# Optimization experiments

Measured on AMD Instinct MI355X. Metric: run time of the kernel, lower is better.

Reference implementation:

```python
import jax, jax.numpy as jnp
import numpy as np

EPS = 1e-08


def setup_inputs() -> dict:
    key = jax.random.key(0)
    k1, k2, k3 = jax.random.split(key, 3)
    N = 4000000
    x = jax.random.normal(k1, (N, 3), dtype=jnp.float32)
    x_gt = jax.random.normal(k2, (N, 3), dtype=jnp.float32)
    weights = jax.random.uniform(k3, (N,), dtype=jnp.float32)
    return {"x": x, "x_gt": x_gt, "weights": weights}


def reference(x, x_gt, weights):
    # weights: [N] -> [N, 1]
    w = weights[:, None]
    weight_sum = w.sum() + EPS
    mu = (w * x).sum(axis=0, keepdims=True) / weight_sum        # [1, 3]
    mu_gt = (w * x_gt).sum(axis=0, keepdims=True) / weight_sum  # [1, 3]
    x_c = x - mu
    x_gt_c = x_gt - mu_gt
    sw = jnp.sqrt(w)
    # H = (sqrt(w)*x_c)^T @ (sqrt(w)*x_gt_c)  -> [3, 3]
    H = jnp.einsum('ni,nj->ij', sw * x_c, sw * x_gt_c)
    U, S, Vt = jnp.linalg.svd(H)
    R = U @ Vt  # == U @ V.T with V = Vt.T
    det_R = jnp.linalg.det(R)
    # Reflection fix: R = U @ diag(1,1,d) @ Vt with d = -1 if det < 0
    d = jnp.where(det_R < 0, -1.0, 1.0).astype(R.dtype)
    F = jnp.array([1.0, 1.0, 0.0], dtype=R.dtype) + jnp.array([0.0, 0.0, 1.0], dtype=R.dtype) * d
    R = (U * F[None, :]) @ Vt
    # x_aligned = (R @ x_gt_c^T)^T + mu = x_gt_c @ R^T + mu
    x_aligned = x_gt_c @ R.T + mu
    return jax.lax.stop_gradient(x_aligned)
```

## Files before the change

### kernel.cpp

```cpp
#include <hip/hip_runtime.h>
#include <math.h>

#define BLK 256

__global__ __launch_bounds__(BLK) void wra_reduce(
    const float* __restrict__ x, const float* __restrict__ g,
    const float* __restrict__ w, float* __restrict__ partials,
    int n4, int n, int ntiles)
{
    __shared__ float4 xs[768];
    __shared__ float4 gs[768];
    __shared__ float4 ws[256];

    float a[16];
#pragma unroll
    for (int i = 0; i < 16; ++i) a[i] = 0.f;

    const float4* __restrict__ x4 = (const float4*)x;
    const float4* __restrict__ g4 = (const float4*)g;
    const float4* __restrict__ w4 = (const float4*)w;

    const int tid = threadIdx.x;
    const int totc = 3 * n4;

    for (int t = blockIdx.x; t < ntiles; t += gridDim.x) {
        const int cb = t * 768;
        const int wb = t * 256;
#pragma unroll
        for (int k = 0; k < 3; ++k) {
            int c = cb + tid + 256 * k;
            float4 xv = make_float4(0.f, 0.f, 0.f, 0.f);
            float4 gv = xv;
            if (c < totc) { xv = x4[c]; gv = g4[c]; }
            xs[tid + 256 * k] = xv;
            gs[tid + 256 * k] = gv;
        }
        {
            int wc = wb + tid;
            ws[tid] = (wc < n4) ? w4[wc] : make_float4(0.f, 0.f, 0.f, 0.f);
        }
        __syncthreads();

        float4 xa = xs[3 * tid + 0], xb = xs[3 * tid + 1], xc = xs[3 * tid + 2];
        float4 ga = gs[3 * tid + 0], gb = gs[3 * tid + 1], gc = gs[3 * tid + 2];
        float4 wv = ws[tid];

        float px[4] = {xa.x, xa.w, xb.z, xc.y};
        float py[4] = {xa.y, xb.x, xb.w, xc.z};
        float pz[4] = {xa.z, xb.y, xc.x, xc.w};
        float qx[4] = {ga.x, ga.w, gb.z, gc.y};
        float qy[4] = {ga.y, gb.x, gb.w, gc.z};
        float qz[4] = {ga.z, gb.y, gc.x, gc.w};
        float wt[4] = {wv.x, wv.y, wv.z, wv.w};
#pragma unroll
        for (int k = 0; k < 4; ++k) {
            float wk = wt[k];
            float wpx = wk * px[k], wpy = wk * py[k], wpz = wk * pz[k];
            a[0] += wk;
            a[1] += wpx;         a[2] += wpy;         a[3] += wpz;
            a[4] += wk * qx[k];  a[5] += wk * qy[k];  a[6] += wk * qz[k];
            a[7]  += wpx * qx[k]; a[8]  += wpx * qy[k]; a[9]  += wpx * qz[k];
            a[10] += wpy * qx[k]; a[11] += wpy * qy[k]; a[12] += wpy * qz[k];
            a[13] += wpz * qx[k]; a[14] += wpz * qy[k]; a[15] += wpz * qz[k];
        }
        __syncthreads();
    }

    if (blockIdx.x == 0 && tid == 0) {
        for (int r = n4 * 4; r < n; ++r) {
            float wk = w[r];
            float X = x[3 * r], Y = x[3 * r + 1], Z = x[3 * r + 2];
            float Gx = g[3 * r], Gy = g[3 * r + 1], Gz = g[3 * r + 2];
            float wpx = wk * X, wpy = wk * Y, wpz = wk * Z;
            a[0] += wk;
            a[1] += wpx;      a[2] += wpy;      a[3] += wpz;
            a[4] += wk * Gx;  a[5] += wk * Gy;  a[6] += wk * Gz;
            a[7]  += wpx * Gx; a[8]  += wpx * Gy; a[9]  += wpx * Gz;
            a[10] += wpy * Gx; a[11] += wpy * Gy; a[12] += wpy * Gz;
            a[13] += wpz * Gx; a[14] += wpz * Gy; a[15] += wpz * Gz;
        }
    }

#pragma unroll
    for (int i = 0; i < 16; ++i) {
        float v = a[i];
        for (int off = 32; off > 0; off >>= 1) v += __shfl_down(v, off, 64);
        a[i] = v;
    }
    __shared__ float red[4][16];
    int lane = tid & 63;
    int wid  = tid >> 6;
    if (lane == 0) {
#pragma unroll
        for (int i = 0; i < 16; ++i) red[wid][i] = a[i];
    }
    __syncthreads();
    if (tid < 16) {
        float s = red[0][tid] + red[1][tid] + red[2][tid] + red[3][tid];
        partials[blockIdx.x * 16 + tid] = s;
    }
}

__global__ __launch_bounds__(64) void wra_solve(
    const float* __restrict__ partials, int nb, float* __restrict__ rt)
{
    int lane = threadIdx.x;
    double acc[16];
#pragma unroll
    for (int i = 0; i < 16; ++i) acc[i] = 0.0;
    for (int b = lane; b < nb; b += 64) {
#pragma unroll
        for (int i = 0; i < 16; ++i) acc[i] += (double)partials[b * 16 + i];
    }
#pragma unroll
    for (int i = 0; i < 16; ++i) {
        double v = acc[i];
        for (int off = 32; off > 0; off >>= 1) v += __shfl_down(v, off, 64);
        acc[i] = v;
    }
    if (lane != 0) return;

    double Sw = acc[0];
    double Sx[3] = {acc[1], acc[2], acc[3]};
    double Sg[3] = {acc[4], acc[5], acc[6]};
    double Hr[3][3];
    for (int i = 0; i < 3; ++i)
        for (int j = 0; j < 3; ++j) Hr[i][j] = acc[7 + i * 3 + j];

    double W = Sw + 1e-8;
    double mu[3], mg[3];
    for (int i = 0; i < 3; ++i) { mu[i] = Sx[i] / W; mg[i] = Sg[i] / W; }

    double H[3][3];
    for (int i = 0; i < 3; ++i)
        for (int j = 0; j < 3; ++j)
            H[i][j] = Hr[i][j] - mu[i] * Sg[j] - mg[j] * Sx[i] + mu[i] * mg[j] * Sw;

    double A[3][3];
    for (int i = 0; i < 3; ++i)
        for (int j = 0; j < 3; ++j) {
            double s = 0.0;
            for (int k = 0; k < 3; ++k) s += H[k][i] * H[k][j];
            A[i][j] = s;
        }

    double V[3][3] = {{1,0,0},{0,1,0},{0,0,1}};
    const int pr[3] = {0, 0, 1}, qr[3] = {1, 2, 2};
    for (int sweep = 0; sweep < 25; ++sweep) {
        for (int r = 0; r < 3; ++r) {
            int p = pr[r], q = qr[r];
            double apq = A[p][q];
            if (fabs(apq) < 1e-30) continue;
            double tau = (A[q][q] - A[p][p]) / (2.0 * apq);
            double t = (tau >= 0 ? 1.0 : -1.0) / (fabs(tau) + sqrt(1.0 + tau * tau));
            double c = 1.0 / sqrt(1.0 + t * t), s = t * c;
            for (int k = 0; k < 3; ++k) {
                double akp = A[k][p], akq = A[k][q];
                A[k][p] = c * akp - s * akq;
                A[k][q] = s * akp + c * akq;
            }
            for (int k = 0; k < 3; ++k) {
                double apk = A[p][k], aqk = A[q][k];
                A[p][k] = c * apk - s * aqk;
                A[q][k] = s * apk + c * aqk;
            }
            for (int k = 0; k < 3; ++k) {
                double vkp = V[k][p], vkq = V[k][q];
                V[k][p] = c * vkp - s * vkq;
                V[k][q] = s * vkp + c * vkq;
            }
        }
    }
    double lam[3] = {A[0][0], A[1][1], A[2][2]};

    int idx[3] = {0, 1, 2};
    if (lam[idx[0]] < lam[idx[1]]) { int t = idx[0]; idx[0] = idx[1]; idx[1] = t; }
    if (lam[idx[1]] < lam[idx[2]]) { int t = idx[1]; idx[1] = idx[2]; idx[2] = t; }
    if (lam[idx[0]] < lam[idx[1]]) { int t = idx[0]; idx[0] = idx[1]; idx[1] = t; }

    double Vs[3][3], U[3][3];
    for (int k = 0; k < 3; ++k) {
        int c0 = idx[k];
        double l = lam[c0] > 1e-30 ? lam[c0] : 1e-30;
        double inv = 1.0 / sqrt(l);
        for (int i = 0; i < 3; ++i) Vs[i][k] = V[i][c0];
        for (int i = 0; i < 3; ++i) {
            double s = 0.0;
            for (int j = 0; j < 3; ++j) s += H[i][j] * Vs[j][k];
            U[i][k] = s * inv;
        }
    }

    double detH = H[0][0] * (H[1][1] * H[2][2] - H[1][2] * H[2][1])
                - H[0][1] * (H[1][0] * H[2][2] - H[1][2] * H[2][0])
                + H[0][2] * (H[1][0] * H[2][1] - H[1][1] * H[2][0]);
    double d = (detH < 0.0) ? -1.0 : 1.0;

    double R[3][3];
    for (int i = 0; i < 3; ++i)
        for (int j = 0; j < 3; ++j)
            R[i][j] = U[i][0] * Vs[j][0] + U[i][1] * Vs[j][1] + d * U[i][2] * Vs[j][2];

    double tv[3];
    for (int i = 0; i < 3; ++i)
        tv[i] = mu[i] - (R[i][0] * mg[0] + R[i][1] * mg[1] + R[i][2] * mg[2]);

    for (int i = 0; i < 3; ++i)
        for (int j = 0; j < 3; ++j) rt[i * 3 + j] = (float)R[i][j];
    for (int i = 0; i < 3; ++i) rt[9 + i] = (float)tv[i];
}

__global__ __launch_bounds__(BLK) void wra_apply(
    const float* __restrict__ g, const float* __restrict__ rt,
    float* __restrict__ out, int n4, int n, int ntiles)
{
    __shared__ float4 buf[768];

    float R00 = rt[0], R01 = rt[1], R02 = rt[2];
    float R10 = rt[3], R11 = rt[4], R12 = rt[5];
    float R20 = rt[6], R21 = rt[7], R22 = rt[8];
    float t0 = rt[9], t1 = rt[10], t2 = rt[11];

    const float4* __restrict__ g4 = (const float4*)g;
    float4* __restrict__ o4 = (float4*)out;

    const int tid = threadIdx.x;
    const int totc = 3 * n4;

    for (int t = blockIdx.x; t < ntiles; t += gridDim.x) {
        const int cb = t * 768;
#pragma unroll
        for (int k = 0; k < 3; ++k) {
            int c = cb + tid + 256 * k;
            if (c < totc) buf[tid + 256 * k] = g4[c];
        }
        __syncthreads();

        float4 ga = buf[3 * tid + 0], gb = buf[3 * tid + 1], gc = buf[3 * tid + 2];
        float qx0 = ga.x, qy0 = ga.y, qz0 = ga.z;
        float qx1 = ga.w, qy1 = gb.x, qz1 = gb.y;
        float qx2 = gb.z, qy2 = gb.w, qz2 = gc.x;
        float qx3 = gc.y, qy3 = gc.z, qz3 = gc.w;

        float ox0 = R00*qx0 + R01*qy0 + R02*qz0 + t0;
        float oy0 = R10*qx0 + R11*qy0 + R12*qz0 + t1;
        float oz0 = R20*qx0 + R21*qy0 + R22*qz0 + t2;
        float ox1 = R00*qx1 + R01*qy1 + R02*qz1 + t0;
        float oy1 = R10*qx1 + R11*qy1 + R12*qz1 + t1;
        float oz1 = R20*qx1 + R21*qy1 + R22*qz1 + t2;
        float ox2 = R00*qx2 + R01*qy2 + R02*qz2 + t0;
        float oy2 = R10*qx2 + R11*qy2 + R12*qz2 + t1;
        float oz2 = R20*qx2 + R21*qy2 + R22*qz2 + t2;
        float ox3 = R00*qx3 + R01*qy3 + R02*qz3 + t0;
        float oy3 = R10*qx3 + R11*qy3 + R12*qz3 + t1;
        float oz3 = R20*qx3 + R21*qy3 + R22*qz3 + t2;

        buf[3 * tid + 0] = make_float4(ox0, oy0, oz0, ox1);
        buf[3 * tid + 1] = make_float4(oy1, oz1, ox2, oy2);
        buf[3 * tid + 2] = make_float4(oz2, ox3, oy3, oz3);
        __syncthreads();

#pragma unroll
        for (int k = 0; k < 3; ++k) {
            int c = cb + tid + 256 * k;
            if (c < totc) o4[c] = buf[tid + 256 * k];
        }
        __syncthreads();
    }

    int gtid = blockIdx.x * blockDim.x + threadIdx.x;
    int gstr = gridDim.x * blockDim.x;
    for (int r = n4 * 4 + gtid; r < n; r += gstr) {
        float Gx = g[3 * r], Gy = g[3 * r + 1], Gz = g[3 * r + 2];
        out[3 * r + 0] = R00 * Gx + R01 * Gy + R02 * Gz + t0;
        out[3 * r + 1] = R10 * Gx + R11 * Gy + R12 * Gz + t1;
        out[3 * r + 2] = R20 * Gx + R21 * Gy + R22 * Gz + t2;
    }
}

extern "C" void kernel_launch(void* const* d_in, const int* in_sizes, int n_in,
                              void* d_out, int out_size, void* d_ws, size_t ws_size,
                              hipStream_t stream)
{
    const float* x = (const float*)d_in[0];
    const float* g = (const float*)d_in[1];
    const float* w = (const float*)d_in[2];
    float* out = (float*)d_out;

    int n = in_sizes[2];
    int n4 = n / 4;
    int ntiles = (n4 + 255) / 256;
    if (ntiles < 1) ntiles = 1;

    int nbr = 1024;
    int maxnb = (int)((ws_size / sizeof(float) - 12) / 16);
    if (nbr > maxnb) nbr = maxnb;
    if (nbr > ntiles) nbr = ntiles;
    if (nbr < 1) nbr = 1;

    float* partials = (float*)d_ws;
    float* rt = partials + (size_t)nbr * 16;

    wra_reduce<<<nbr, BLK, 0, stream>>>(x, g, w, partials, n4, n, ntiles);
    wra_solve<<<1, 64, 0, stream>>>(partials, nbr, rt);

    int nba = ntiles < 2048 ? ntiles : 2048;
    wra_apply<<<nba, BLK, 0, stream>>>(g, rt, out, n4, n, ntiles);
}
```

Measured before the change: 56.88 us.

## Prefetch next tile into registers while computing current tile from shared memory

Restructures the grid-stride reduction loop so the global loads for the next tile are issued into registers before the current tile is processed from shared memory, then stored to shared memory after a barrier. This software pipelining is meant to hide global memory latency behind the accumulation math in a bandwidth-bound reduction. It costs extra registers for the prefetch buffers, which may lower occupancy, and adds a second barrier per iteration.

```diff
diff --git a/kernel.cpp b/kernel.cpp
--- a/kernel.cpp
+++ b/kernel.cpp
@@ -22,48 +22,75 @@
 
     const int tid = threadIdx.x;
     const int totc = 3 * n4;
-
-    for (int t = blockIdx.x; t < ntiles; t += gridDim.x) {
+    const float4 z4 = make_float4(0.f, 0.f, 0.f, 0.f);
+
+    int t = blockIdx.x;
+    {
+        float4 rx[3], rg[3], rw;
         const int cb = t * 768;
-        const int wb = t * 256;
 #pragma unroll
         for (int k = 0; k < 3; ++k) {
             int c = cb + tid + 256 * k;
-            float4 xv = make_float4(0.f, 0.f, 0.f, 0.f);
-            float4 gv = xv;
-            if (c < totc) { xv = x4[c]; gv = g4[c]; }
-            xs[tid + 256 * k] = xv;
-            gs[tid + 256 * k] = gv;
-        }
+            rx[k] = z4; rg[k] = z4;
+            if (c < totc) { rx[k] = x4[c]; rg[k] = g4[c]; }
+        }
+        int wc = t * 256 + tid;
+        rw = (wc < n4) ? w4[wc] : z4;
+#pragma unroll
+        for (int k = 0; k < 3; ++k) { xs[tid + 256 * k] = rx[k]; gs[tid + 256 * k] = rg[k]; }
+        ws[tid] = rw;
+    }
+    __syncthreads();
+
+    while (t < ntiles) {
+        const int tn = t + gridDim.x;
+        const bool havenext = (tn < ntiles);
+        float4 px[3], pg[3], pw;
+        if (havenext) {
+            const int cb = tn * 768;
+#pragma unroll
+            for (int k = 0; k < 3; ++k) {
+                int c = cb + tid + 256 * k;
+                px[k] = z4; pg[k] = z4;
+                if (c < totc) { px[k] = x4[c]; pg[k] = g4[c]; }
+            }
+            int wc = tn * 256 + tid;
+            pw = (wc < n4) ? w4[wc] : z4;
+        }
+
         {
-            int wc = wb + tid;
-            ws[tid] = (wc < n4) ? w4[wc] : make_float4(0.f, 0.f, 0.f, 0.f);
-        }
-        __syncthreads();
-
-        float4 xa = xs[3 * tid + 0], xb = xs[3 * tid + 1], xc = xs[3 * tid + 2];
-        float4 ga = gs[3 * tid + 0], gb = gs[3 * tid + 1], gc = gs[3 * tid + 2];
-        float4 wv = ws[tid];
-
-        float px[4] = {xa.x, xa.w, xb.z, xc.y};
-        float py[4] = {xa.y, xb.x, xb.w, xc.z};
-        float pz[4] = {xa.z, xb.y, xc.x, xc.w};
-        float qx[4] = {ga.x, ga.w, gb.z, gc.y};
-        float qy[4] = {ga.y, gb.x, gb.w, gc.z};
-        float qz[4] = {ga.z, gb.y, gc.x, gc.w};
-        float wt[4] = {wv.x, wv.y, wv.z, wv.w};
-#pragma unroll
-        for (int k = 0; k < 4; ++k) {
-            float wk = wt[k];
-            float wpx = wk * px[k], wpy = wk * py[k], wpz = wk * pz[k];
-            a[0] += wk;
-            a[1] += wpx;         a[2] += wpy;         a[3] += wpz;
-            a[4] += wk * qx[k];  a[5] += wk * qy[k];  a[6] += wk * qz[k];
-            a[7]  += wpx * qx[k]; a[8]  += wpx * qy[k]; a[9]  += wpx * qz[k];
-            a[10] += wpy * qx[k]; a[11] += wpy * qy[k]; a[12] += wpy * qz[k];
-            a[13] += wpz * qx[k]; a[14] += wpz * qy[k]; a[15] += wpz * qz[k];
-        }
-        __syncthreads();
+            float4 xa = xs[3 * tid + 0], xb = xs[3 * tid + 1], xc = xs[3 * tid + 2];
+            float4 ga = gs[3 * tid + 0], gb = gs[3 * tid + 1], gc = gs[3 * tid + 2];
+            float4 wv = ws[tid];
+
+            float pxc[4] = {xa.x, xa.w, xb.z, xc.y};
+            float pyc[4] = {xa.y, xb.x, xb.w, xc.z};
+            float pzc[4] = {xa.z, xb.y, xc.x, xc.w};
+            float qxc[4] = {ga.x, ga.w, gb.z, gc.y};
+            float qyc[4] = {ga.y, gb.x, gb.w, gc.z};
+            float qzc[4] = {ga.z, gb.y, gc.x, gc.w};
+            float wt[4]  = {wv.x, wv.y, wv.z, wv.w};
+#pragma unroll
+            for (int k = 0; k < 4; ++k) {
+                float wk = wt[k];
+                float wpx = wk * pxc[k], wpy = wk * pyc[k], wpz = wk * pzc[k];
+                a[0] += wk;
+                a[1] += wpx;          a[2] += wpy;          a[3] += wpz;
+                a[4] += wk * qxc[k];  a[5] += wk * qyc[k];  a[6] += wk * qzc[k];
+                a[7]  += wpx * qxc[k]; a[8]  += wpx * qyc[k]; a[9]  += wpx * qzc[k];
+                a[10] += wpy * qxc[k]; a[11] += wpy * qyc[k]; a[12] += wpy * qzc[k];
+                a[13] += wpz * qxc[k]; a[14] += wpz * qyc[k]; a[15] += wpz * qzc[k];
+            }
+        }
+        __syncthreads();
+
+        if (havenext) {
+#pragma unroll
+            for (int k = 0; k < 3; ++k) { xs[tid + 256 * k] = px[k]; gs[tid + 256 * k] = pg[k]; }
+            ws[tid] = pw;
+        }
+        __syncthreads();
+        t = tn;
     }
 
     if (blockIdx.x == 0 && tid == 0) {
```

Measured after the change: 56.81 us. No clear change (-0.1%).

## Load reduce inputs directly into registers with nontemporal loads and 2x unroll

Applied to the files above, without the earlier changes.

The reduction kernel drops its shared-memory staging and barriers. Each thread now loads its own three float4 of x and g plus one float4 of w straight into registers, with a two-iteration unroll to keep more loads in flight. x and w use nontemporal loads while g uses normal loads, presumably so g stays in cache for the apply pass. The apply kernel writes its output with nontemporal stores, and the reduce grid grows from 1024 to 2048 blocks. The trade-off is strided per-thread 48-byte accesses, which coalesce less well than the old staged loads.

```diff
diff --git a/kernel.cpp b/kernel.cpp
--- a/kernel.cpp
+++ b/kernel.cpp
@@ -1,76 +1,86 @@
 #include <hip/hip_runtime.h>
 #include <math.h>
 
+typedef float f32x4 __attribute__((ext_vector_type(4)));
+
 #define BLK 256
+
+__device__ __forceinline__ void accum4(
+    float a[16], f32x4 xa, f32x4 xb, f32x4 xc,
+    f32x4 ga, f32x4 gb, f32x4 gc, f32x4 wv)
+{
+    float px[4] = {xa.x, xa.w, xb.z, xc.y};
+    float py[4] = {xa.y, xb.x, xb.w, xc.z};
+    float pz[4] = {xa.z, xb.y, xc.x, xc.w};
+    float qx[4] = {ga.x, ga.w, gb.z, gc.y};
+    float qy[4] = {ga.y, gb.x, gb.w, gc.z};
+    float qz[4] = {ga.z, gb.y, gc.x, gc.w};
+    float wt[4] = {wv.x, wv.y, wv.z, wv.w};
+#pragma unroll
+    for (int k = 0; k < 4; ++k) {
+        float wk = wt[k];
+        float wpx = wk * px[k], wpy = wk * py[k], wpz = wk * pz[k];
+        a[0] += wk;
+        a[1] += wpx;         a[2] += wpy;         a[3] += wpz;
+        a[4] += wk * qx[k];  a[5] += wk * qy[k];  a[6] += wk * qz[k];
+        a[7]  += wpx * qx[k]; a[8]  += wpx * qy[k]; a[9]  += wpx * qz[k];
+        a[10] += wpy * qx[k]; a[11] += wpy * qy[k]; a[12] += wpy * qz[k];
+        a[13] += wpz * qx[k]; a[14] += wpz * qy[k]; a[15] += wpz * qz[k];
+    }
+}
 
 __global__ __launch_bounds__(BLK) void wra_reduce(
     const float* __restrict__ x, const float* __restrict__ g,
     const float* __restrict__ w, float* __restrict__ partials,
-    int n4, int n, int ntiles)
-{
-    __shared__ float4 xs[768];
-    __shared__ float4 gs[768];
-    __shared__ float4 ws[256];
-
+    int n4, int n)
+{
     float a[16];
 #pragma unroll
     for (int i = 0; i < 16; ++i) a[i] = 0.f;
 
-    const float4* __restrict__ x4 = (const float4*)x;
-    const float4* __restrict__ g4 = (const float4*)g;
-    const float4* __restrict__ w4 = (const float4*)w;
-
-    const int tid = threadIdx.x;
-    const int totc = 3 * n4;
-
-    for (int t = blockIdx.x; t < ntiles; t += gridDim.x) {
-        const int cb = t * 768;
-        const int wb = t * 256;
-#pragma unroll
-        for (int k = 0; k < 3; ++k) {
-            int c = cb + tid + 256 * k;
-            float4 xv = make_float4(0.f, 0.f, 0.f, 0.f);
-            float4 gv = xv;
-            if (c < totc) { xv = x4[c]; gv = g4[c]; }
-            xs[tid + 256 * k] = xv;
-            gs[tid + 256 * k] = gv;
-        }
-        {
-            int wc = wb + tid;
-            ws[tid] = (wc < n4) ? w4[wc] : make_float4(0.f, 0.f, 0.f, 0.f);
-        }
-        __syncthreads();
-
-        float4 xa = xs[3 * tid + 0], xb = xs[3 * tid + 1], xc = xs[3 * tid + 2];
-        float4 ga = gs[3 * tid + 0], gb = gs[3 * tid + 1], gc = gs[3 * tid + 2];
-        float4 wv = ws[tid];
-
-        float px[4] = {xa.x, xa.w, xb.z, xc.y};
-        float py[4] = {xa.y, xb.x, xb.w, xc.z};
-        float pz[4] = {xa.z, xb.y, xc.x, xc.w};
-        float qx[4] = {ga.x, ga.w, gb.z, gc.y};
-        float qy[4] = {ga.y, gb.x, gb.w, gc.z};
-        float qz[4] = {ga.z, gb.y, gc.x, gc.w};
-        float wt[4] = {wv.x, wv.y, wv.z, wv.w};
-#pragma unroll
-        for (int k = 0; k < 4; ++k) {
-            float wk = wt[k];
-            float wpx = wk * px[k], wpy = wk * py[k], wpz = wk * pz[k];
-            a[0] += wk;
-            a[1] += wpx;         a[2] += wpy;         a[3] += wpz;
-            a[4] += wk * qx[k];  a[5] += wk * qy[k];  a[6] += wk * qz[k];
-            a[7]  += wpx * qx[k]; a[8]  += wpx * qy[k]; a[9]  += wpx * qz[k];
-            a[10] += wpy * qx[k]; a[11] += wpy * qy[k]; a[12] += wpy * qz[k];
-            a[13] += wpz * qx[k]; a[14] += wpz * qy[k]; a[15] += wpz * qz[k];
-        }
-        __syncthreads();
-    }
-
-    if (blockIdx.x == 0 && tid == 0) {
+    const f32x4* __restrict__ x4 = (const f32x4*)x;
+    const f32x4* __restrict__ g4 = (const f32x4*)g;
+    const f32x4* __restrict__ w4 = (const f32x4*)w;
+
+    int tid = blockIdx.x * blockDim.x + threadIdx.x;
+    int stride = gridDim.x * blockDim.x;
+
+    int i = tid;
+    for (; i + stride < n4; i += 2 * stride) {
+        int j = i + stride;
+        f32x4 xa0 = __builtin_nontemporal_load(&x4[3*i+0]);
+        f32x4 xb0 = __builtin_nontemporal_load(&x4[3*i+1]);
+        f32x4 xc0 = __builtin_nontemporal_load(&x4[3*i+2]);
+        f32x4 ga0 = g4[3*i+0];
+        f32x4 gb0 = g4[3*i+1];
+        f32x4 gc0 = g4[3*i+2];
+        f32x4 wv0 = __builtin_nontemporal_load(&w4[i]);
+        f32x4 xa1 = __builtin_nontemporal_load(&x4[3*j+0]);
+        f32x4 xb1 = __builtin_nontemporal_load(&x4[3*j+1]);
+        f32x4 xc1 = __builtin_nontemporal_load(&x4[3*j+2]);
+        f32x4 ga1 = g4[3*j+0];
+        f32x4 gb1 = g4[3*j+1];
+        f32x4 gc1 = g4[3*j+2];
+        f32x4 wv1 = __builtin_nontemporal_load(&w4[j]);
+        accum4(a, xa0, xb0, xc0, ga0, gb0, gc0, wv0);
+        accum4(a, xa1, xb1, xc1, ga1, gb1, gc1, wv1);
+    }
+    for (; i < n4; i += stride) {
+        f32x4 xa = __builtin_nontemporal_load(&x4[3*i+0]);
+        f32x4 xb = __builtin_nontemporal_load(&x4[3*i+1]);
+        f32x4 xc = __builtin_nontemporal_load(&x4[3*i+2]);
+        f32x4 ga = g4[3*i+0];
+        f32x4 gb = g4[3*i+1];
+        f32x4 gc = g4[3*i+2];
+        f32x4 wv = __builtin_nontemporal_load(&w4[i]);
+        accum4(a, xa, xb, xc, ga, gb, gc, wv);
+    }
+
+    if (blockIdx.x == 0 && threadIdx.x == 0) {
         for (int r = n4 * 4; r < n; ++r) {
             float wk = w[r];
-            float X = x[3 * r], Y = x[3 * r + 1], Z = x[3 * r + 2];
-            float Gx = g[3 * r], Gy = g[3 * r + 1], Gz = g[3 * r + 2];
+            float X = x[3*r], Y = x[3*r+1], Z = x[3*r+2];
+            float Gx = g[3*r], Gy = g[3*r+1], Gz = g[3*r+2];
             float wpx = wk * X, wpy = wk * Y, wpz = wk * Z;
             a[0] += wk;
             a[1] += wpx;      a[2] += wpy;      a[3] += wpz;
@@ -82,22 +92,23 @@
     }
 
 #pragma unroll
-    for (int i = 0; i < 16; ++i) {
-        float v = a[i];
+    for (int i2 = 0; i2 < 16; ++i2) {
+        float v = a[i2];
         for (int off = 32; off > 0; off >>= 1) v += __shfl_down(v, off, 64);
-        a[i] = v;
+        a[i2] = v;
     }
     __shared__ float red[4][16];
-    int lane = tid & 63;
-    int wid  = tid >> 6;
+    int lane = threadIdx.x & 63;
+    int wid  = threadIdx.x >> 6;
     if (lane == 0) {
 #pragma unroll
-        for (int i = 0; i < 16; ++i) red[wid][i] = a[i];
+        for (int i2 = 0; i2 < 16; ++i2) red[wid][i2] = a[i2];
     }
     __syncthreads();
-    if (tid < 16) {
-        float s = red[0][tid] + red[1][tid] + red[2][tid] + red[3][tid];
-        partials[blockIdx.x * 16 + tid] = s;
+    if (threadIdx.x < 16) {
+        float s = red[0][threadIdx.x] + red[1][threadIdx.x]
+                + red[2][threadIdx.x] + red[3][threadIdx.x];
+        partials[blockIdx.x * 16 + threadIdx.x] = s;
     }
 }
 
@@ -214,15 +225,15 @@
     const float* __restrict__ g, const float* __restrict__ rt,
     float* __restrict__ out, int n4, int n, int ntiles)
 {
-    __shared__ float4 buf[768];
+    __shared__ f32x4 buf[768];
 
     float R00 = rt[0], R01 = rt[1], R02 = rt[2];
     float R10 = rt[3], R11 = rt[4], R12 = rt[5];
     float R20 = rt[6], R21 = rt[7], R22 = rt[8];
     float t0 = rt[9], t1 = rt[10], t2 = rt[11];
 
-    const float4* __restrict__ g4 = (const float4*)g;
-    float4* __restrict__ o4 = (float4*)out;
+    const f32x4* __restrict__ g4 = (const f32x4*)g;
+    f32x4* __restrict__ o4 = (f32x4*)out;
 
     const int tid = threadIdx.x;
     const int totc = 3 * n4;
@@ -236,34 +247,35 @@
         }
         __syncthreads();
 
-        float4 ga = buf[3 * tid + 0], gb = buf[3 * tid + 1], gc = buf[3 * tid + 2];
+        f32x4 ga = buf[3 * tid + 0], gb = buf[3 * tid + 1], gc = buf[3 * tid + 2];
         float qx0 = ga.x, qy0 = ga.y, qz0 = ga.z;
         float qx1 = ga.w, qy1 = gb.x, qz1 = gb.y;
         float qx2 = gb.z, qy2 = gb.w, qz2 = gc.x;
         float qx3 = gc.y, qy3 = gc.z, qz3 = gc.w;
 
-        float ox0 = R00*qx0 + R01*qy0 + R02*qz0 + t0;
-        float oy0 = R10*qx0 + R11*qy0 + R12*qz0 + t1;
-        float oz0 = R20*qx0 + R21*qy0 + R22*qz0 + t2;
-        float ox1 = R00*qx1 + R01*qy1 + R02*qz1 + t0;
-        float oy1 = R10*qx1 + R11*qy1 + R12*qz1 + t1;
-        float oz1 = R20*qx1 + R21*qy1 + R22*qz1 + t2;
-        float ox2 = R00*qx2 + R01*qy2 + R02*qz2 + t0;
-        float oy2 = R10*qx2 + R11*qy2 + R12*qz2 + t1;
-        float oz2 = R20*qx2 + R21*qy2 + R22*qz2 + t2;
-        float ox3 = R00*qx3 + R01*qy3 + R02*qz3 + t0;
-        float oy3 = R10*qx3 + R11*qy3 + R12*qz3 + t1;
-        float oz3 = R20*qx3 + R21*qy3 + R22*qz3 + t2;
-
-        buf[3 * tid + 0] = make_float4(ox0, oy0, oz0, ox1);
-        buf[3 * tid + 1] = make_float4(oy1, oz1, ox2, oy2);
-        buf[3 * tid + 2] = make_float4(oz2, ox3, oy3, oz3);
+        f32x4 r0, r1, r2;
+        r0.x = R00*qx0 + R01*qy0 + R02*qz0 + t0;
+        r0.y = R10*qx0 + R11*qy0 + R12*qz0 + t1;
+        r0.z = R20*qx0 + R21*qy0 + R22*qz0 + t2;
+        r0.w = R00*qx1 + R01*qy1 + R02*qz1 + t0;
+        r1.x = R10*qx1 + R11*qy1 + R12*qz1 + t1;
+        r1.y = R20*qx1 + R21*qy1 + R22*qz1 + t2;
+        r1.z = R00*qx2 + R01*qy2 + R02*qz2 + t0;
+        r1.w = R10*qx2 + R11*qy2 + R12*qz2 + t1;
+        r2.x = R20*qx2 + R21*qy2 + R22*qz2 + t2;
+        r2.y = R00*qx3 + R01*qy3 + R02*qz3 + t0;
+        r2.z = R10*qx3 + R11*qy3 + R12*qz3 + t1;
+        r2.w = R20*qx3 + R21*qy3 + R22*qz3 + t2;
+
+        buf[3 * tid + 0] = r0;
+        buf[3 * tid + 1] = r1;
+        buf[3 * tid + 2] = r2;
         __syncthreads();
 
 #pragma unroll
         for (int k = 0; k < 3; ++k) {
             int c = cb + tid + 256 * k;
-            if (c < totc) o4[c] = buf[tid + 256 * k];
+            if (c < totc) __builtin_nontemporal_store(buf[tid + 256 * k], &o4[c]);
         }
         __syncthreads();
     }
@@ -271,10 +283,10 @@
     int gtid = blockIdx.x * blockDim.x + threadIdx.x;
     int gstr = gridDim.x * blockDim.x;
     for (int r = n4 * 4 + gtid; r < n; r += gstr) {
-        float Gx = g[3 * r], Gy = g[3 * r + 1], Gz = g[3 * r + 2];
-        out[3 * r + 0] = R00 * Gx + R01 * Gy + R02 * Gz + t0;
-        out[3 * r + 1] = R10 * Gx + R11 * Gy + R12 * Gz + t1;
-        out[3 * r + 2] = R20 * Gx + R21 * Gy + R22 * Gz + t2;
+        float Gx = g[3*r], Gy = g[3*r+1], Gz = g[3*r+2];
+        out[3*r+0] = R00*Gx + R01*Gy + R02*Gz + t0;
+        out[3*r+1] = R10*Gx + R11*Gy + R12*Gz + t1;
+        out[3*r+2] = R20*Gx + R21*Gy + R22*Gz + t2;
     }
 }
 
@@ -292,16 +304,18 @@
     int ntiles = (n4 + 255) / 256;
     if (ntiles < 1) ntiles = 1;
 
-    int nbr = 1024;
+    int nbr = 2048;
     int maxnb = (int)((ws_size / sizeof(float) - 12) / 16);
     if (nbr > maxnb) nbr = maxnb;
-    if (nbr > ntiles) nbr = ntiles;
+    int need = (n4 + BLK - 1) / BLK;
+    if (need < 1) need = 1;
+    if (nbr > need) nbr = need;
     if (nbr < 1) nbr = 1;
 
     float* partials = (float*)d_ws;
     float* rt = partials + (size_t)nbr * 16;
 
-    wra_reduce<<<nbr, BLK, 0, stream>>>(x, g, w, partials, n4, n, ntiles);
+    wra_reduce<<<nbr, BLK, 0, stream>>>(x, g, w, partials, n4, n);
     wra_solve<<<1, 64, 0, stream>>>(partials, nbr, rt);
 
     int nba = ntiles < 2048 ? ntiles : 2048;
```

After: 61.67 us. 8.4% more time.
